# Optimization experiments

Measured on AMD Instinct MI355X. Metric: run time of the kernel, lower is better.

The kernel has to match this reference:

```python
import jax, jax.numpy as jnp
import numpy as np

B, T, K, N, D, E = 64, 12, 4, 400, 64, 16


def _ln(x, g, b, eps):
    m = jnp.mean(x, axis=-1, keepdims=True)
    v = jnp.var(x, axis=-1, keepdims=True)
    return (x - m) * jax.lax.rsqrt(v + eps) * g + b


def setup_inputs() -> dict:
    key = jax.random.key(0)
    ks = jax.random.split(key, 8)
    return {
        "x": jax.random.normal(ks[0], (B, T, N, D), jnp.float32),
        "selected_x": jax.random.normal(ks[1], (B, T, K, N, D), jnp.float32),
        "selected_relevant_values": jax.random.normal(ks[2], (T, K), jnp.float32),
        "selected_indices": jax.random.randint(ks[3], (T, K), 0, T),
        "node_embeddings": jax.random.normal(ks[4], (N, E), jnp.float32),
        "time_embeddings": jax.random.normal(ks[5], (T, E), jnp.float32),
        "ln_emb_g": jnp.ones((E,), jnp.float32),
        "ln_emb_b": jnp.zeros((E,), jnp.float32),
        "weights_pool": 0.1 * jax.random.normal(ks[6], (E, 2, D, D), jnp.float32),
        "bias_pool": 0.1 * jax.random.normal(ks[7], (E, D), jnp.float32),
        "gcn_ln_g": jnp.ones((D,), jnp.float32),
        "gcn_ln_b": jnp.zeros((D,), jnp.float32),
        "out_ln_g": jnp.ones((D,), jnp.float32),
        "out_ln_b": jnp.zeros((D,), jnp.float32),
    }


def reference(x, selected_x, selected_relevant_values, selected_indices,
              node_embeddings, time_embeddings, ln_emb_g, ln_emb_b,
              weights_pool, bias_pool, gcn_ln_g, gcn_ln_b, out_ln_g, out_ln_b):
    # full_embeddings: (N, T, E)
    full = node_embeddings[:, None, :] + time_embeddings[None, :, :]
    triu = jnp.triu(jnp.ones((K, K), jnp.float32))  # mask for j >= i blocks
    eyeK = jnp.eye(K, dtype=jnp.float32)

    def per_t(femb, rv, idx, sx):
        # femb: (N,E), rv: (K,), idx: (K,), sx: (B,K,N,D)
        embt = _ln(femb, ln_emb_g, ln_emb_b, 1e-12)  # dropout is identity in eval
        supports = jax.nn.softmax(embt @ embt.T, axis=1)  # (N,N)
        diagm = jnp.diag(jnp.diagonal(supports))          # diag(supports) as matrix
        # cross_graph blocks: (i==j): supports + rv[j]*diagm ; (j>i): rv[j]*diagm ; else 0
        cg = (triu[:, :, None, None] * rv[None, :, None, None] * diagm
              + eyeK[:, :, None, None] * supports)        # (K,K,N,N)
        cross = cg.transpose(0, 2, 1, 3).reshape(N * K, N * K)
        # (B,K,N,D) -> (B,N,K,D) -> (B, N*K, D)
        sxr = sx.transpose(0, 2, 1, 3).reshape(-1, N * K, D)
        semb = full[:, idx, :].reshape(N * K, E)          # (NK,E)
        # GCN with cheb_k=2: supports set = [I, cross]; I @ x == x
        weights = jnp.einsum('nd,dkio->nkio', semb, weights_pool)  # (NK,2,D,D)
        bias = semb @ bias_pool                                    # (NK,D)
        xg1 = jnp.einsum('nm,bmc->bnc', cross, sxr)                # (B,NK,D)
        x_g = jnp.stack([sxr, xg1], axis=2)                        # (B,NK,2,D)
        h = jnp.einsum('bnki,nkio->bno', x_g, weights) + bias
        return _ln(h, gcn_ln_g, gcn_ln_b, 1e-5)                    # (B,NK,D)

    out = jax.vmap(per_t)(jnp.swapaxes(full, 0, 1),
                          selected_relevant_values,
                          selected_indices,
                          jnp.swapaxes(selected_x, 0, 1))          # (T,B,NK,D)
    out = out.reshape(T, -1, N, K, D).transpose(1, 0, 2, 4, 3).mean(-1)  # (B,T,N,D)
    out = _ln(out, out_ln_g, out_ln_b, 1e-5)
    return out + selected_x.mean(2)
```

## Files before the change

### kernel.cpp

```cpp
#include <hip/hip_runtime.h>
#include <hip/hip_bf16.h>

#define TB 64
#define TT 12
#define TK 4
#define TN 400
#define TD 64
#define TE 16
#define QP 1664
#define MP 416

typedef unsigned short ushort_t;
typedef __attribute__((ext_vector_type(8))) short short8v;
typedef __attribute__((ext_vector_type(4))) float float4v;
typedef __attribute__((ext_vector_type(4))) unsigned short us4;
typedef __attribute__((ext_vector_type(8))) unsigned short us8;

__device__ __forceinline__ float bf2f(ushort_t u) {
    union { unsigned int i; float f; } v; v.i = ((unsigned int)u) << 16; return v.f;
}
__device__ __forceinline__ ushort_t f2bf(float f) {
    union { float f; unsigned int i; } v; v.f = f;
    unsigned int u = v.i;
    return (ushort_t)((u + 0x7fffu + ((u >> 16) & 1u)) >> 16);
}

__global__ void k_embt(const float* __restrict__ node, const float* __restrict__ timee,
                       const float* __restrict__ g, const float* __restrict__ b,
                       float* __restrict__ embt) {
    int id = blockIdx.x * blockDim.x + threadIdx.x;
    if (id >= TT * TN) return;
    int t = id / TN, n = id % TN;
    float v[TE];
    float s = 0.f;
#pragma unroll
    for (int e = 0; e < TE; e++) { v[e] = node[n * TE + e] + timee[t * TE + e]; s += v[e]; }
    float mean = s * (1.f / TE);
    float s2 = 0.f;
#pragma unroll
    for (int e = 0; e < TE; e++) { float d = v[e] - mean; s2 += d * d; }
    float rstd = rsqrtf(s2 * (1.f / TE) + 1e-12f);
#pragma unroll
    for (int e = 0; e < TE; e++) embt[(size_t)id * TE + e] = (v[e] - mean) * rstd * g[e] + b[e];
}

__global__ __launch_bounds__(128) void k_supports(const float* __restrict__ embt,
                                                  ushort_t* __restrict__ supN,
                                                  float* __restrict__ diag) {
    int t = blockIdx.x / TN, n = blockIdx.x % TN;
    int tid = threadIdx.x;
    __shared__ float row[TE];
    __shared__ float red[128];
    if (tid < TE) row[tid] = embt[((size_t)t * TN + n) * TE + tid];
    __syncthreads();
    float l[4];
    float lmax = -1e30f;
#pragma unroll
    for (int it = 0; it < 4; it++) {
        int m = tid + it * 128;
        float d = -1e30f;
        if (m < TN) {
            d = 0.f;
            const float* er = &embt[((size_t)t * TN + m) * TE];
#pragma unroll
            for (int e = 0; e < TE; e++) d += row[e] * er[e];
        }
        l[it] = d;
        lmax = fmaxf(lmax, d);
    }
    red[tid] = lmax; __syncthreads();
    for (int s = 64; s > 0; s >>= 1) { if (tid < s) red[tid] = fmaxf(red[tid], red[tid + s]); __syncthreads(); }
    float mx = red[0]; __syncthreads();
    float lsum = 0.f;
#pragma unroll
    for (int it = 0; it < 4; it++) {
        int m = tid + it * 128;
        if (m < TN) { l[it] = expf(l[it] - mx); lsum += l[it]; }
    }
    red[tid] = lsum; __syncthreads();
    for (int s = 64; s > 0; s >>= 1) { if (tid < s) red[tid] += red[tid + s]; __syncthreads(); }
    float inv = 1.f / red[0];
    ushort_t* srow = supN + ((size_t)t * TN + n) * MP;
#pragma unroll
    for (int it = 0; it < 4; it++) {
        int m = tid + it * 128;
        if (m < TN) {
            float v = l[it] * inv;
            srow[m] = f2bf(v);
            if (m == n) diag[t * TN + n] = v;
        }
    }
    if (tid < MP - TN) srow[TN + tid] = 0;
}

__global__ __launch_bounds__(256) void k_mix(const float* __restrict__ emb, const float* __restrict__ wp,
                                             const float* __restrict__ bp, float* __restrict__ M,
                                             float* __restrict__ bias) {
    int n = blockIdx.x;
    __shared__ float ev[TE];
    if (threadIdx.x < TE) ev[threadIdx.x] = emb[n * TE + threadIdx.x];
    __syncthreads();
    for (int idx = threadIdx.x; idx < 128 * TD; idx += 256) {
        float s = 0.f;
#pragma unroll
        for (int e = 0; e < TE; e++) s += ev[e] * wp[(size_t)e * 8192 + idx];
        M[(size_t)n * 8192 + idx] = s;
    }
    if (threadIdx.x < TD) {
        float s = 0.f;
#pragma unroll
        for (int e = 0; e < TE; e++) s += ev[e] * bp[e * TD + threadIdx.x];
        bias[n * TD + threadIdx.x] = s;
    }
}

__global__ __launch_bounds__(256) void k_prepX(const float* __restrict__ sx, ushort_t* __restrict__ Xg,
                                               int t0, size_t tstride) {
    const int qt = blockIdx.x;
    const int bct = blockIdx.y;
    const int t = t0 + blockIdx.z;
    ushort_t* Xgt = Xg + (size_t)blockIdx.z * tstride;
    const int tid = threadIdx.x;
    __shared__ ushort_t Ls[64][264];
    for (int idx = tid; idx < 4096; idx += 256) {
        int qr = idx >> 6, u = idx & 63;
        int q = qt * 64 + qr;
        us4 z;
        if (q < 1600) {
            int bc = bct * 256 + u * 4;
            int b = bc >> 6, c = bc & 63;
            const float4 v = *(const float4*)&sx[((((size_t)b * TT + t) * TK + (q & 3)) * TN + (q >> 2)) * TD + c];
            z[0] = f2bf(v.x); z[1] = f2bf(v.y); z[2] = f2bf(v.z); z[3] = f2bf(v.w);
        } else { z[0] = 0; z[1] = 0; z[2] = 0; z[3] = 0; }
        *(us4*)&Ls[qr][u * 4] = z;
    }
    __syncthreads();
    const int g = tid >> 3, seg = tid & 7;
    for (int p = 0; p < 8; ++p) {
        int bcl = p * 32 + g;
        us8 wv;
#pragma unroll
        for (int s = 0; s < 8; ++s) wv[s] = Ls[seg * 8 + s][bcl];
        *(us8*)&Xgt[(size_t)(bct * 256 + bcl) * QP + qt * 64 + seg * 8] = wv;
    }
}

#define ISSUE(ii, mm0) do { \
    ra0 = *(const us4*)&supt[(size_t)(n0 + (tid >> 3)) * MP + (mm0) + (tid & 7) * 4]; \
    { int idx_ = tid + 256; ra1 = *(const us4*)&supt[(size_t)(n0 + (idx_ >> 3)) * MP + (mm0) + (idx_ & 7) * 4]; } \
    if (tid < 128) { int idx_ = tid + 512; ra2 = *(const us4*)&supt[(size_t)(n0 + (idx_ >> 3)) * MP + (mm0) + (idx_ & 7) * 4]; } \
    rx0 = *(const us8*)&Xgt[(size_t)(bc0 + (tid >> 2)) * QP + (ii) * 400 + (mm0) + (tid & 3) * 8]; \
    { int idx_ = tid + 256; rx1 = *(const us8*)&Xgt[(size_t)(bc0 + (idx_ >> 2)) * QP + (ii) * 400 + (mm0) + (idx_ & 3) * 8]; } \
} while (0)

#define COMMIT(buf) do { \
    *(us4*)&As[buf][tid >> 3][(tid & 7) * 4] = ra0; \
    { int idx_ = tid + 256; *(us4*)&As[buf][idx_ >> 3][(idx_ & 7) * 4] = ra1; } \
    if (tid < 128) { int idx_ = tid + 512; *(us4*)&As[buf][idx_ >> 3][(idx_ & 7) * 4] = ra2; } \
    *(us8*)&Xs[buf][tid >> 2][(tid & 3) * 8] = rx0; \
    { int idx_ = tid + 256; *(us8*)&Xs[buf][idx_ >> 2][(idx_ & 3) * 8] = rx1; } \
} while (0)

__global__ __launch_bounds__(256, 2) void k_xg1m(const ushort_t* __restrict__ Xg, const ushort_t* __restrict__ supN,
                                                 const float* __restrict__ diag, const float* __restrict__ rv,
                                                 ushort_t* __restrict__ xg1, int t0, size_t xgstride, size_t x1stride) {
    const int ntile = blockIdx.x;
    const int bct = blockIdx.y;
    const int tz = blockIdx.z;
    const int t = t0 + tz;
    const ushort_t* Xgt = Xg + (size_t)tz * xgstride;
    ushort_t* x1t = xg1 + (size_t)tz * x1stride;
    const int tid = threadIdx.x;
    const int w = tid >> 6, l = tid & 63;
    const int lr = l & 15, lk = (l >> 4) * 8;
    const int n0 = ntile * 80, bc0 = bct * 128;
    __shared__ ushort_t As[2][80][40];
    __shared__ ushort_t Xs[2][128][40];
    const ushort_t* supt = supN + (size_t)t * TN * MP;
    const float4 rv4 = *(const float4*)&rv[t * TK];
    const float rvj[4] = {rv4.x, rv4.y, rv4.z, rv4.w};
    float4v rs[5][2] = {};
    float4v acc[5][2] = {};
    us4 ra0, ra1, ra2;
    us8 rx0, rx1;

    ISSUE(3, 0);
    COMMIT(0);
    __syncthreads();
    int cur = 0;
#pragma unroll 1
    for (int c = 0; c < 52; ++c) {
        const int i = 3 - c / 13;
        const int m0 = (c % 13) * 32;
        if (c + 1 < 52) {
            const int i2 = 3 - (c + 1) / 13;
            const int m02 = ((c + 1) % 13) * 32;
            ISSUE(i2, m02);
        }
        short8v bfr[2];
#pragma unroll
        for (int ct = 0; ct < 2; ++ct) bfr[ct] = *(const short8v*)&Xs[cur][w * 32 + ct * 16 + lr][lk];
#pragma unroll
        for (int fr = 0; fr < 5; ++fr) {
            short8v a = *(const short8v*)&As[cur][fr * 16 + lr][lk];
#pragma unroll
            for (int ct = 0; ct < 2; ++ct)
                acc[fr][ct] = __builtin_amdgcn_mfma_f32_16x16x32_bf16(a, bfr[ct], acc[fr][ct], 0, 0, 0);
        }
        if (m0 + 32 > n0 && m0 < n0 + 80) {
            const float rvi = rvj[i];
#pragma unroll
            for (int fr = 0; fr < 5; ++fr)
#pragma unroll
                for (int r = 0; r < 4; ++r) {
                    const int nb = n0 + fr * 16 + ((l >> 4) << 2) + r;
                    const int d = nb - m0;
                    if ((unsigned)d < 32u) {
#pragma unroll
                        for (int ct = 0; ct < 2; ++ct)
                            rs[fr][ct][r] += rvi * bf2f(Xs[cur][w * 32 + ct * 16 + lr][d]);
                    }
                }
        }
        if ((c % 13) == 12) {
#pragma unroll
            for (int fr = 0; fr < 5; ++fr) {
                const int nb = n0 + fr * 16 + ((l >> 4) << 2);
                const float4 dg4 = *(const float4*)&diag[t * TN + nb];
                const float dg[4] = {dg4.x, dg4.y, dg4.z, dg4.w};
#pragma unroll
                for (int ct = 0; ct < 2; ++ct) {
                    const int bc = bc0 + w * 32 + ct * 16 + lr;
#pragma unroll
                    for (int r = 0; r < 4; ++r) {
                        float val = acc[fr][ct][r] + dg[r] * rs[fr][ct][r];
                        x1t[(size_t)(i * TN + nb + r) * 4096 + bc] = f2bf(val);
                    }
                    acc[fr][ct] = (float4v){0.f, 0.f, 0.f, 0.f};
                }
            }
        }
        if (c + 1 < 52) COMMIT(cur ^ 1);
        __syncthreads();
        cur ^= 1;
    }
}

__global__ __launch_bounds__(256, 2) void k_head10(const float* __restrict__ sx, const ushort_t* __restrict__ xg1,
                                                   const float* __restrict__ Mn, const float* __restrict__ Mt,
                                                   const float* __restrict__ bn, const float* __restrict__ bt,
                                                   const int* __restrict__ idxs,
                                                   const float* __restrict__ gg, const float* __restrict__ gb,
                                                   const float* __restrict__ og, const float* __restrict__ ob,
                                                   float* __restrict__ out, int t0, size_t x1stride) {
    const int n = blockIdx.x;
    const int tz = blockIdx.y;
    const int t = t0 + tz;
    const ushort_t* x1t = xg1 + (size_t)tz * x1stride;
    const int tid = threadIdx.x;
    const int tx = tid & 15, ty = tid >> 4;
    const int o0 = tx * 4, b0 = ty * 4;
    __shared__ __align__(16) float Ml[64][68];
    __shared__ __align__(16) float Zl[64][68];
    float accout[4][4] = {};
    float g4[4], gb4[4];
#pragma unroll
    for (int c = 0; c < 4; c++) { g4[c] = gg[o0 + c]; gb4[c] = gb[o0 + c]; }
    const float* mnp = Mn + (size_t)n * 8192;

    for (int k = 0; k < TK; k++) {
        int tau = idxs[t * TK + k];
        const float* mtp = Mt + (size_t)tau * 8192;
        float acch[4][4] = {};
#pragma unroll 1
        for (int ih = 0; ih < 2; ih++) {
            for (int idx = tid; idx < 1024; idx += 256) {
                int il = idx >> 4, o4 = idx & 15;
                const float4 a = *(const float4*)&mnp[(ih * 64 + il) * 64 + o4 * 4];
                const float4 c = *(const float4*)&mtp[(ih * 64 + il) * 64 + o4 * 4];
                float4 r; r.x = a.x + c.x; r.y = a.y + c.y; r.z = a.z + c.z; r.w = a.w + c.w;
                *(float4*)&Ml[il][o4 * 4] = r;
            }
            if (ih == 0) {
                for (int idx = tid; idx < 1024; idx += 256) {
                    int b = idx >> 4, c4 = idx & 15;
                    const float4 v = *(const float4*)&sx[((((size_t)b * TT + t) * TK + k) * TN + n) * TD + c4 * 4];
                    *(float4*)&Zl[b][c4 * 4] = v;
                }
            } else {
                for (int idx = tid; idx < 512; idx += 256) {
                    int b = idx >> 3, s = idx & 7;
                    us8 xv = *(const us8*)&x1t[((size_t)n * TK + k) * 4096 + b * 64 + s * 8];
                    float* zp = &Zl[b][s * 8];
#pragma unroll
                    for (int q = 0; q < 8; q++) zp[q] = bf2f(xv[q]);
                }
            }
            __syncthreads();
            for (int i0 = 0; i0 < 64; i0 += 4) {
                float m[4][4];
#pragma unroll
                for (int q = 0; q < 4; q++) {
                    float4 mv = *(const float4*)&Ml[i0 + q][o0];
                    m[q][0] = mv.x; m[q][1] = mv.y; m[q][2] = mv.z; m[q][3] = mv.w;
                }
#pragma unroll
                for (int r = 0; r < 4; r++) {
                    float4 zv = *(const float4*)&Zl[b0 + r][i0];
                    float z[4] = {zv.x, zv.y, zv.z, zv.w};
#pragma unroll
                    for (int q = 0; q < 4; q++)
#pragma unroll
                        for (int c = 0; c < 4; c++) acch[r][c] += z[q] * m[q][c];
                }
            }
            __syncthreads();
        }
#pragma unroll
        for (int c = 0; c < 4; c++) {
            float bias = bn[n * TD + o0 + c] + bt[tau * TD + o0 + c];
#pragma unroll
            for (int r = 0; r < 4; r++) acch[r][c] += bias;
        }
#pragma unroll
        for (int r = 0; r < 4; r++) {
            float s1 = acch[r][0] + acch[r][1] + acch[r][2] + acch[r][3];
            float s2 = acch[r][0] * acch[r][0] + acch[r][1] * acch[r][1] +
                       acch[r][2] * acch[r][2] + acch[r][3] * acch[r][3];
#pragma unroll
            for (int mk = 1; mk < 16; mk <<= 1) { s1 += __shfl_xor(s1, mk); s2 += __shfl_xor(s2, mk); }
            float mean = s1 * (1.f / TD);
            float var  = s2 * (1.f / TD) - mean * mean;
            float rstd = rsqrtf(var + 1e-5f);
#pragma unroll
            for (int c = 0; c < 4; c++) accout[r][c] += (acch[r][c] - mean) * rstd * g4[c] + gb4[c];
        }
    }

    float og4[4], ob4[4];
#pragma unroll
    for (int c = 0; c < 4; c++) { og4[c] = og[o0 + c]; ob4[c] = ob[o0 + c]; }
#pragma unroll
    for (int r = 0; r < 4; r++) {
        float pre[4];
#pragma unroll
        for (int c = 0; c < 4; c++) pre[c] = accout[r][c] * 0.25f;
        float s1 = pre[0] + pre[1] + pre[2] + pre[3];
        float s2 = pre[0] * pre[0] + pre[1] * pre[1] + pre[2] * pre[2] + pre[3] * pre[3];
#pragma unroll
        for (int mk2 = 1; mk2 < 16; mk2 <<= 1) { s1 += __shfl_xor(s1, mk2); s2 += __shfl_xor(s2, mk2); }
        float mean = s1 * (1.f / TD);
        float var  = s2 * (1.f / TD) - mean * mean;
        float rstd = rsqrtf(var + 1e-5f);
        float mk[4] = {0, 0, 0, 0};
        const float* sxp = &sx[(((size_t)(b0 + r) * TT + t) * TK) * TN * TD + (size_t)n * TD + o0];
#pragma unroll
        for (int k = 0; k < TK; k++) {
            float4 sv = *(const float4*)&sxp[(size_t)k * TN * TD];
            mk[0] += sv.x; mk[1] += sv.y; mk[2] += sv.z; mk[3] += sv.w;
        }
        float4 res;
        res.x = (pre[0] - mean) * rstd * og4[0] + ob4[0] + 0.25f * mk[0];
        res.y = (pre[1] - mean) * rstd * og4[1] + ob4[1] + 0.25f * mk[1];
        res.z = (pre[2] - mean) * rstd * og4[2] + ob4[2] + 0.25f * mk[2];
        res.w = (pre[3] - mean) * rstd * og4[3] + ob4[3] + 0.25f * mk[3];
        *reinterpret_cast<float4*>(&out[(((size_t)(b0 + r) * TT + t) * TN + n) * TD + o0]) = res;
    }
}

extern "C" void kernel_launch(void* const* d_in, const int* in_sizes, int n_in,
                              void* d_out, int out_size, void* d_ws, size_t ws_size,
                              hipStream_t stream) {
    (void)in_sizes; (void)n_in; (void)out_size;
    const float* sx    = (const float*)d_in[1];
    const float* rv    = (const float*)d_in[2];
    const int*   idxs  = (const int*)d_in[3];
    const float* node  = (const float*)d_in[4];
    const float* timee = (const float*)d_in[5];
    const float* leg   = (const float*)d_in[6];
    const float* leb   = (const float*)d_in[7];
    const float* wp    = (const float*)d_in[8];
    const float* bp    = (const float*)d_in[9];
    const float* gg    = (const float*)d_in[10];
    const float* gb    = (const float*)d_in[11];
    const float* og    = (const float*)d_in[12];
    const float* ob    = (const float*)d_in[13];
    float* out = (float*)d_out;

    char* w = (char*)d_ws;
    size_t off = 0;
    auto alloc = [&](size_t bytes) { size_t o = off; off = (off + bytes + 255) & ~(size_t)255; return o; };
    float*    embt = (float*)(w + alloc((size_t)TT * TN * TE * 4));
    ushort_t* supN = (ushort_t*)(w + alloc((size_t)TT * TN * MP * 2));
    float*    diag = (float*)(w + alloc((size_t)TT * TN * 4));
    float*    Mn   = (float*)(w + alloc((size_t)TN * 8192 * 4));
    float*    Mt   = (float*)(w + alloc((size_t)TT * 8192 * 4));
    float*    bn   = (float*)(w + alloc((size_t)TN * TD * 4));
    float*    bt   = (float*)(w + alloc((size_t)TT * TD * 4));
    const size_t xg_elems = (size_t)4096 * QP;
    const size_t x1_elems = (size_t)1600 * 4096;
    const size_t small_end = off;
    const bool full = ws_size >= small_end + 12 * (xg_elems + x1_elems) * 2 + 1024;
    const int nt = full ? TT : 1;
    ushort_t* Xg = (ushort_t*)(w + alloc((size_t)nt * xg_elems * 2));
    ushort_t* x1 = (ushort_t*)(w + alloc((size_t)nt * x1_elems * 2));

    k_embt<<<dim3((TT * TN + 255) / 256), 256, 0, stream>>>(node, timee, leg, leb, embt);
    k_supports<<<dim3(TT * TN), 128, 0, stream>>>(embt, supN, diag);
    k_mix<<<dim3(TN), 256, 0, stream>>>(node, wp, bp, Mn, bn);
    k_mix<<<dim3(TT), 256, 0, stream>>>(timee, wp, bp, Mt, bt);
    if (full) {
        k_prepX<<<dim3(26, 16, TT), 256, 0, stream>>>(sx, Xg, 0, xg_elems);
        k_xg1m<<<dim3(5, 32, TT), 256, 0, stream>>>(Xg, supN, diag, rv, x1, 0, xg_elems, x1_elems);
        k_head10<<<dim3(TN, TT), 256, 0, stream>>>(sx, x1, Mn, Mt, bn, bt, idxs, gg, gb, og, ob, out, 0, x1_elems);
    } else {
        for (int t = 0; t < TT; ++t) {
            k_prepX<<<dim3(26, 16, 1), 256, 0, stream>>>(sx, Xg, t, 0);
            k_xg1m<<<dim3(5, 32, 1), 256, 0, stream>>>(Xg, supN, diag, rv, x1, t, 0, 0);
            k_head10<<<dim3(TN, 1), 256, 0, stream>>>(sx, x1, Mn, Mt, bn, bt, idxs, gg, gb, og, ob, out, t, 0);
        }
    }
}
```

Measured before the change: 727.4 us.

## Software-pipeline global loads into registers in the per-node GCN apply kernel

```diff
diff --git a/kernel.cpp b/kernel.cpp
--- a/kernel.cpp
+++ b/kernel.cpp
@@ -267,73 +267,125 @@
 #pragma unroll
     for (int c = 0; c < 4; c++) { g4[c] = gg[o0 + c]; gb4[c] = gb[o0 + c]; }
     const float* mnp = Mn + (size_t)n * 8192;
-
-    for (int k = 0; k < TK; k++) {
-        int tau = idxs[t * TK + k];
-        const float* mtp = Mt + (size_t)tau * 8192;
-        float acch[4][4] = {};
+    int taus[4];
+#pragma unroll
+    for (int k = 0; k < 4; k++) taus[k] = idxs[t * TK + k];
+
+    float4 rmn[4], rmt[4], rz[4];
+    us8 rx[2];
+
+#define H_ISSUE(kk, ih) do { \
+    const float* mtp_ = Mt + (size_t)taus[kk] * 8192; \
+    _Pragma("unroll") \
+    for (int j = 0; j < 4; ++j) { \
+        int idx_ = tid + j * 256; \
+        int il_ = idx_ >> 4, o4_ = idx_ & 15; \
+        rmn[j] = *(const float4*)&mnp[((ih) * 64 + il_) * 64 + o4_ * 4]; \
+        rmt[j] = *(const float4*)&mtp_[((ih) * 64 + il_) * 64 + o4_ * 4]; \
+    } \
+    if ((ih) == 0) { \
+        _Pragma("unroll") \
+        for (int j = 0; j < 4; ++j) { \
+            int idx_ = tid + j * 256; \
+            int b_ = idx_ >> 4, c4_ = idx_ & 15; \
+            rz[j] = *(const float4*)&sx[((((size_t)b_ * TT + t) * TK + (kk)) * TN + n) * TD + c4_ * 4]; \
+        } \
+    } else { \
+        _Pragma("unroll") \
+        for (int j = 0; j < 2; ++j) { \
+            int idx_ = tid + j * 256; \
+            int b_ = idx_ >> 3, s_ = idx_ & 7; \
+            rx[j] = *(const us8*)&x1t[((size_t)n * TK + (kk)) * 4096 + b_ * 64 + s_ * 8]; \
+        } \
+    } \
+} while (0)
+
+#define H_COMMIT(ih) do { \
+    _Pragma("unroll") \
+    for (int j = 0; j < 4; ++j) { \
+        int idx_ = tid + j * 256; \
+        int il_ = idx_ >> 4, o4_ = idx_ & 15; \
+        float4 r_; r_.x = rmn[j].x + rmt[j].x; r_.y = rmn[j].y + rmt[j].y; \
+        r_.z = rmn[j].z + rmt[j].z; r_.w = rmn[j].w + rmt[j].w; \
+        *(float4*)&Ml[il_][o4_ * 4] = r_; \
+    } \
+    if ((ih) == 0) { \
+        _Pragma("unroll") \
+        for (int j = 0; j < 4; ++j) { \
+            int idx_ = tid + j * 256; \
+            int b_ = idx_ >> 4, c4_ = idx_ & 15; \
+            *(float4*)&Zl[b_][c4_ * 4] = rz[j]; \
+        } \
+    } else { \
+        _Pragma("unroll") \
+        for (int j = 0; j < 2; ++j) { \
+            int idx_ = tid + j * 256; \
+            int b_ = idx_ >> 3, s_ = idx_ & 7; \
+            float* zp_ = &Zl[b_][s_ * 8]; \
+            _Pragma("unroll") \
+            for (int q_ = 0; q_ < 8; ++q_) zp_[q_] = bf2f(rx[j][q_]); \
+        } \
+    } \
+} while (0)
+
+    H_ISSUE(0, 0);
+    H_COMMIT(0);
+    __syncthreads();
+
+    float acch[4][4] = {};
 #pragma unroll 1
-        for (int ih = 0; ih < 2; ih++) {
-            for (int idx = tid; idx < 1024; idx += 256) {
-                int il = idx >> 4, o4 = idx & 15;
-                const float4 a = *(const float4*)&mnp[(ih * 64 + il) * 64 + o4 * 4];
-                const float4 c = *(const float4*)&mtp[(ih * 64 + il) * 64 + o4 * 4];
-                float4 r; r.x = a.x + c.x; r.y = a.y + c.y; r.z = a.z + c.z; r.w = a.w + c.w;
-                *(float4*)&Ml[il][o4 * 4] = r;
+    for (int p = 0; p < 8; ++p) {
+        const int k = p >> 1, ih = p & 1;
+        if (p + 1 < 8) {
+            const int k2 = (p + 1) >> 1, ih2 = (p + 1) & 1;
+            if (ih2 == 0) H_ISSUE(k2, 0); else H_ISSUE(k2, 1);
+        }
+        for (int i0 = 0; i0 < 64; i0 += 4) {
+            float m[4][4];
+#pragma unroll
+            for (int q = 0; q < 4; q++) {
+                float4 mv = *(const float4*)&Ml[i0 + q][o0];
+                m[q][0] = mv.x; m[q][1] = mv.y; m[q][2] = mv.z; m[q][3] = mv.w;
             }
-            if (ih == 0) {
-                for (int idx = tid; idx < 1024; idx += 256) {
-                    int b = idx >> 4, c4 = idx & 15;
-                    const float4 v = *(const float4*)&sx[((((size_t)b * TT + t) * TK + k) * TN + n) * TD + c4 * 4];
-                    *(float4*)&Zl[b][c4 * 4] = v;
-                }
-            } else {
-                for (int idx = tid; idx < 512; idx += 256) {
-                    int b = idx >> 3, s = idx & 7;
-                    us8 xv = *(const us8*)&x1t[((size_t)n * TK + k) * 4096 + b * 64 + s * 8];
-                    float* zp = &Zl[b][s * 8];
-#pragma unroll
-                    for (int q = 0; q < 8; q++) zp[q] = bf2f(xv[q]);
+#pragma unroll
+            for (int r = 0; r < 4; r++) {
+                float4 zv = *(const float4*)&Zl[b0 + r][i0];
+                float z[4] = {zv.x, zv.y, zv.z, zv.w};
+#pragma unroll
+                for (int q = 0; q < 4; q++)
+#pragma unroll
+                    for (int c = 0; c < 4; c++) acch[r][c] += z[q] * m[q][c];
+            }
+        }
+        if (ih == 1) {
+#pragma unroll
+            for (int c = 0; c < 4; c++) {
+                float bias = bn[n * TD + o0 + c] + bt[taus[k] * TD + o0 + c];
+#pragma unroll
+                for (int r = 0; r < 4; r++) acch[r][c] += bias;
+            }
+#pragma unroll
+            for (int r = 0; r < 4; r++) {
+                float s1 = acch[r][0] + acch[r][1] + acch[r][2] + acch[r][3];
+                float s2 = acch[r][0] * acch[r][0] + acch[r][1] * acch[r][1] +
+                           acch[r][2] * acch[r][2] + acch[r][3] * acch[r][3];
+#pragma unroll
+                for (int mk = 1; mk < 16; mk <<= 1) { s1 += __shfl_xor(s1, mk); s2 += __shfl_xor(s2, mk); }
+                float mean = s1 * (1.f / TD);
+                float var  = s2 * (1.f / TD) - mean * mean;
+                float rstd = rsqrtf(var + 1e-5f);
+#pragma unroll
+                for (int c = 0; c < 4; c++) {
+                    accout[r][c] += (acch[r][c] - mean) * rstd * g4[c] + gb4[c];
+                    acch[r][c] = 0.f;
                 }
             }
+        }
+        __syncthreads();
+        if (p + 1 < 8) {
+            const int ih2 = (p + 1) & 1;
+            if (ih2 == 0) H_COMMIT(0); else H_COMMIT(1);
             __syncthreads();
-            for (int i0 = 0; i0 < 64; i0 += 4) {
-                float m[4][4];
-#pragma unroll
-                for (int q = 0; q < 4; q++) {
-                    float4 mv = *(const float4*)&Ml[i0 + q][o0];
-                    m[q][0] = mv.x; m[q][1] = mv.y; m[q][2] = mv.z; m[q][3] = mv.w;
-                }
-#pragma unroll
-                for (int r = 0; r < 4; r++) {
-                    float4 zv = *(const float4*)&Zl[b0 + r][i0];
-                    float z[4] = {zv.x, zv.y, zv.z, zv.w};
-#pragma unroll
-                    for (int q = 0; q < 4; q++)
-#pragma unroll
-                        for (int c = 0; c < 4; c++) acch[r][c] += z[q] * m[q][c];
-                }
-            }
-            __syncthreads();
-        }
-#pragma unroll
-        for (int c = 0; c < 4; c++) {
-            float bias = bn[n * TD + o0 + c] + bt[tau * TD + o0 + c];
-#pragma unroll
-            for (int r = 0; r < 4; r++) acch[r][c] += bias;
-        }
-#pragma unroll
-        for (int r = 0; r < 4; r++) {
-            float s1 = acch[r][0] + acch[r][1] + acch[r][2] + acch[r][3];
-            float s2 = acch[r][0] * acch[r][0] + acch[r][1] * acch[r][1] +
-                       acch[r][2] * acch[r][2] + acch[r][3] * acch[r][3];
-#pragma unroll
-            for (int mk = 1; mk < 16; mk <<= 1) { s1 += __shfl_xor(s1, mk); s2 += __shfl_xor(s2, mk); }
-            float mean = s1 * (1.f / TD);
-            float var  = s2 * (1.f / TD) - mean * mean;
-            float rstd = rsqrtf(var + 1e-5f);
-#pragma unroll
-            for (int c = 0; c < 4; c++) accout[r][c] += (acch[r][c] - mean) * rstd * g4[c] + gb4[c];
         }
     }
 
```

New measurement: 803.5 us. 1.1x slower.
